# Kernel optimization log

Measured on AMD Instinct MI355X. Metric: run time of the kernel, lower is better.

The kernel has to match this reference:

```python
import jax, jax.numpy as jnp
import numpy as np

B, N, E = 2, 2048, 1024
H, D = 16, 64


def setup_inputs() -> dict:
    key = jax.random.key(0)
    k1, k2, k3 = jax.random.split(key, 3)
    x = jax.random.normal(k1, (B, N, E), dtype=jnp.float32)
    Wqkv = jax.random.normal(k2, (3 * H * D, E), dtype=jnp.float32) * 0.02
    bqkv = jnp.zeros((3 * H * D,), dtype=jnp.float32)
    Wout = jax.random.normal(k3, (E, H * D), dtype=jnp.float32) * 0.02
    bout = jnp.zeros((E,), dtype=jnp.float32)
    return {"x": x, "Wqkv": Wqkv, "bqkv": bqkv, "Wout": Wout, "bout": bout}


def reference(x, Wqkv, bqkv, Wout, bout):
    b, n, _ = x.shape
    scale = D ** (-0.5)
    # qkv projection: [b, n, 3*h*d], interpreted as (h, d, qkv) per einops pattern
    qkv = (x @ Wqkv.T + bqkv).reshape(b, n, H, D, 3)
    q = jnp.transpose(qkv[..., 0], (0, 2, 1, 3))  # [b, h, n, d]
    k = jnp.transpose(qkv[..., 1], (0, 2, 1, 3))
    v = jnp.transpose(qkv[..., 2], (0, 2, 1, 3))
    att = jnp.einsum('bhid,bhjd->bhij', q, k) * scale  # [b, h, n, n]
    causal = jnp.tril(jnp.ones((n, n), dtype=bool))
    att = jnp.where(causal, att, -jnp.inf)
    att = jax.nn.softmax(att, axis=-1)
    out = jnp.einsum('bhij,bhjd->bhid', att, v)  # [b, h, n, d]
    out = jnp.transpose(out, (0, 2, 1, 3)).reshape(b, n, H * D)
    return out @ Wout.T + bout
```

## Files before the change

### kernel.cpp

```cpp
#include <hip/hip_runtime.h>
#include <hip/hip_bf16.h>

#define B_ 2
#define N_ 2048
#define E_ 1024
#define H_ 16
#define D_ 64
#define M_ 4096
#define HD_ 1024
#define NT_ 3072

using f32x4  = __attribute__((ext_vector_type(4))) float;
using f32x16 = __attribute__((ext_vector_type(16))) float;
using bf16x8 = __attribute__((ext_vector_type(8))) short;

static __device__ __forceinline__ unsigned short f2bf(float f) {
  union { float f; unsigned u; } v; v.f = f;
  unsigned r = v.u + 0x7FFF + ((v.u >> 16) & 1);
  return (unsigned short)(r >> 16);
}
static __device__ __forceinline__ float bf2f(short s) {
  union { unsigned u; float f; } v; v.u = ((unsigned)(unsigned short)s) << 16; return v.f;
}

static __device__ __forceinline__ void gld16(const void* g, void* l) {
  __builtin_amdgcn_global_load_lds(
      (const __attribute__((address_space(1))) unsigned int*)g,
      (__attribute__((address_space(3))) unsigned int*)l, 16, 0, 0);
}

static __device__ __forceinline__ unsigned cvtpk(float lo, float hi) {
  unsigned r;
  asm("v_cvt_pk_bf16_f32 %0, %1, %2" : "=v"(r) : "v"(lo), "v"(hi));
  return r;
}
static __device__ __forceinline__ void pl32swap(unsigned& a, unsigned& b) {
  asm("v_permlane32_swap_b32 %0, %1" : "+v"(a), "+v"(b));
}

static __device__ __forceinline__ int gswz(int row) {
  return ((row >> 1) & 3) ^ ((row >> 3) & 1);
}


__global__ void k_cvt_x(const float* __restrict__ x, unsigned short* __restrict__ xb) {
  int t = blockIdx.x * 256 + threadIdx.x;
  float4 v = reinterpret_cast<const float4*>(x)[t];
  ushort4 o;
  o.x = f2bf(v.x); o.y = f2bf(v.y); o.z = f2bf(v.z); o.w = f2bf(v.w);
  reinterpret_cast<ushort4*>(xb)[t] = o;
}

__global__ void k_cvt_wqkv(const float* __restrict__ w, const float* __restrict__ bsrc,
                           unsigned short* __restrict__ wb, float* __restrict__ br) {
  int t = blockIdx.x * 256 + threadIdx.x;
  int r = t >> 8;
  int c = (t & 255) * 4;
  int kind = r >> 10, hd = r & 1023;
  int h = hd >> 6, d = hd & 63;
  int rin = h * 192 + d * 3 + kind;
  float s = (kind == 0) ? 0.125f * 1.4426950408889634f : 1.0f;
  float4 v = *reinterpret_cast<const float4*>(w + (size_t)rin * E_ + c);
  ushort4 o;
  o.x = f2bf(v.x * s); o.y = f2bf(v.y * s); o.z = f2bf(v.z * s); o.w = f2bf(v.w * s);
  *reinterpret_cast<ushort4*>(wb + (size_t)r * E_ + c) = o;
  if (c == 0) br[r] = bsrc[rin] * s;
}

__global__ void k_cvt_wout(const float* __restrict__ w, unsigned short* __restrict__ wb) {
  int t = blockIdx.x * 256 + threadIdx.x;
  int r = t >> 8;
  int c = (t & 255) * 4;
  float4 v = *reinterpret_cast<const float4*>(w + (size_t)r * HD_ + c);
  ushort4 o;
  o.x = f2bf(v.x); o.y = f2bf(v.y); o.z = f2bf(v.z); o.w = f2bf(v.w);
  *reinterpret_cast<ushort4*>(wb + (size_t)r * HD_ + c) = o;
}

template <int EPI, int BM>
__global__ __launch_bounds__(256, 2) void k_gemm(
    const unsigned short* __restrict__ A,
    const unsigned short* __restrict__ W,
    const float* __restrict__ bias,
    unsigned short* __restrict__ Qo, unsigned short* __restrict__ Ko,
    unsigned short* __restrict__ Vo, float* __restrict__ Fo,
    int M, int Nt, int K)
{
  constexpr int APT = (BM == 128) ? 2 : 1;
  constexpr int NF  = (BM == 128) ? 4 : 2;
  __shared__ unsigned short As[3][BM * 32];
  __shared__ unsigned short Bs[3][128 * 32];
  const int t = threadIdx.x;
  const int w = t >> 6, l = t & 63, lg = l >> 4, lr = l & 15;
  const int wrow0 = (BM == 128) ? (w >> 1) * 64 : 0;
  const int wcol0 = (BM == 128) ? (w & 1) * 64 : w * 32;
  const int row0 = blockIdx.x * BM, col0 = blockIdx.y * 128;
  const int NT = K >> 5;

  f32x4 acc[4][NF] = {};

  auto stage = [&](int b, int k0) {
#pragma unroll
    for (int c = 0; c < APT; ++c) {
      int ci = w * APT + c;
      int row = ci * 16 + (l >> 2);
      int sub = (l & 3) ^ gswz(row);
      gld16(A + (size_t)(row0 + row) * K + k0 + sub * 8,
            (unsigned short*)&As[b][0] + ci * 512);
    }
#pragma unroll
    for (int c = 0; c < 2; ++c) {
      int ci = w * 2 + c;
      int row = ci * 16 + (l >> 2);
      int sub = (l & 3) ^ gswz(row);
      gld16(W + (size_t)(col0 + row) * K + k0 + sub * 8,
            (unsigned short*)&Bs[b][0] + ci * 512);
    }
  };

  stage(0, 0);
  stage(1, 32);

  for (int kt = 0; kt < NT; ++kt) {
    const int ib = kt % 3;
    if (kt + 1 < NT) {
      if constexpr (BM == 128) asm volatile("s_waitcnt vmcnt(4)" ::: "memory");
      else                     asm volatile("s_waitcnt vmcnt(3)" ::: "memory");
    } else {
      asm volatile("s_waitcnt vmcnt(0)" ::: "memory");
    }
    asm volatile("s_barrier" ::: "memory");
    if (kt + 2 < NT) stage((kt + 2) % 3, (kt + 2) * 32);

    bf16x8 af[4], bf[NF];
#pragma unroll
    for (int m = 0; m < 4; ++m) {
      int row = wrow0 + m * 16 + lr;
      af[m] = *reinterpret_cast<const bf16x8*>(
          &As[ib][row * 32 + ((lg ^ gswz(row)) * 8)]);
    }
#pragma unroll
    for (int n = 0; n < NF; ++n) {
      int row = wcol0 + n * 16 + lr;
      bf[n] = *reinterpret_cast<const bf16x8*>(
          &Bs[ib][row * 32 + ((lg ^ gswz(row)) * 8)]);
    }
    __builtin_amdgcn_s_setprio(1);
#pragma unroll
    for (int m = 0; m < 4; ++m)
#pragma unroll
      for (int n = 0; n < NF; ++n)
        acc[m][n] = __builtin_amdgcn_mfma_f32_16x16x32_bf16(af[m], bf[n], acc[m][n], 0, 0, 0);
    __builtin_amdgcn_s_setprio(0);
  }

#pragma unroll
  for (int m = 0; m < 4; ++m) {
#pragma unroll
    for (int n = 0; n < NF; ++n) {
      int col = col0 + wcol0 + n * 16 + lr;
      float bb = bias[col];
#pragma unroll
      for (int rr = 0; rr < 4; ++rr) {
        int ro = row0 + wrow0 + m * 16 + lg * 4 + rr;
        float val = acc[m][n][rr] + bb;
        if (EPI == 0) {
          int kind = col >> 10, hd = col & 1023, h = hd >> 6, d = hd & 63;
          int bi = ro >> 11, ni = ro & 2047;
          unsigned short bv = f2bf(val);
          size_t bh = (size_t)(bi * H_ + h);
          if (kind == 0)      Qo[(bh * N_ + ni) * D_ + d] = bv;
          else if (kind == 1) Ko[(bh * N_ + ni) * D_ + d] = bv;
          else                Vo[bh * (size_t)(D_ * N_) + (size_t)d * N_ + ni] = bv;
        } else {
          Fo[(size_t)ro * HD_ + col] = val;
        }
      }
    }
  }
}

__global__ __launch_bounds__(256, 3) void k_attn(
    const unsigned short* __restrict__ Q,
    const unsigned short* __restrict__ Kg,
    const unsigned short* __restrict__ Vg,
    unsigned short* __restrict__ O,
    unsigned short* __restrict__ Pp,
    float* __restrict__ Pml)
{
  static const int u_qt[24] = {15,15,14,13,12,11,10, 9,   8, 7,14, 6,13, 5,12, 4,   8, 0, 9, 1,10, 2,11, 3};
  static const int u_t0[24] = { 0,16, 0, 0, 0, 0, 0, 0,   0, 0,16, 0,16, 0,16, 0,  16, 0,16, 0,16, 0,16, 0};
  static const int u_ps[24] = {14,15,12,10, 8, 6, 4, 2,   0,-1,13,-1,11,-1, 9,-1,   1,-1, 3,-1, 5,-1, 7,-1};

  __shared__ alignas(16) unsigned short Ks[3][64 * 64];
  __shared__ alignas(16) unsigned short Vs[3][64 * 64];

  const int t = threadIdx.x;
  const int w = t >> 6, l = t & 63;
  const int lq = l & 31;
  const int hi = l >> 5;
  const int bh = blockIdx.x & 31;
  const int u  = blockIdx.x >> 5;
  const int qt = u_qt[u], t0 = u_t0[u], ps = u_ps[u];
  const int q0 = qt * 128;
  const int r0w = q0 + w * 32;
  const int rtop = r0w + 31;
  const bool splitc0 = (ps >= 0) && (t0 == 0);
  const int tendW = splitc0 ? 16 : ((rtop >> 6) + 1);
  const int tendB = splitc0 ? 16 : (((q0 + 127) >> 6) + 1);

  const unsigned short* Qb = Q  + (size_t)bh * (N_ * D_);
  const unsigned short* Kb = Kg + (size_t)bh * (N_ * D_);
  const unsigned short* Vb = Vg + (size_t)bh * (N_ * D_);

  const int pr  = l >> 3;
  const int pswz = ((l & 7) ^ pr) * 8;
  const unsigned short* KsrcB = Kb + pr * D_ + pswz;
  const unsigned short* VsrcB = Vb + pr * N_ + pswz;

  bf16x8 qf[4];
#pragma unroll
  for (int ks = 0; ks < 4; ++ks)
    qf[ks] = *reinterpret_cast<const bf16x8*>(
        Qb + (size_t)(r0w + lq) * D_ + ks * 16 + hi * 8);

  f32x16 oacc[2] = {};
  float lrun = 0.f;

  auto stage = [&](int b, int kt_) {
    const int kv = kt_ * 64;
#pragma unroll
    for (int c = 0; c < 2; ++c) {
      int cb = w * 2 + c;
      gld16(KsrcB + kv * D_ + cb * 512, (unsigned short*)&Ks[b][0] + cb * 512);
      gld16(VsrcB + kv + cb * 8 * N_,   (unsigned short*)&Vs[b][0] + cb * 512);
    }
  };

  stage(0, t0);
  if (t0 + 1 < tendB) stage(1, t0 + 1);

  for (int kt = t0; kt < tendB; ++kt) {
    const int ib = (kt - t0) % 3;
    if (kt + 1 < tendB) asm volatile("s_waitcnt vmcnt(4)" ::: "memory");
    else                asm volatile("s_waitcnt vmcnt(0)" ::: "memory");
    asm volatile("s_barrier" ::: "memory");
    if (kt + 2 < tendB) stage((kt - t0 + 2) % 3, kt + 2);

    if (kt < tendW) {
      const int kv0 = kt * 64;
      bf16x8 kf[2][4], vf[2][4];
#pragma unroll
      for (int ct = 0; ct < 2; ++ct)
#pragma unroll
        for (int ks = 0; ks < 4; ++ks) {
          int row = ct * 32 + lq;
          kf[ct][ks] = *reinterpret_cast<const bf16x8*>(
              &Ks[ib][row * 64 + (((ks * 2 + hi) ^ (lq & 7)) * 8)]);
        }
#pragma unroll
      for (int dt = 0; dt < 2; ++dt)
#pragma unroll
        for (int j = 0; j < 4; ++j) {
          int row = dt * 32 + lq;
          vf[dt][j] = *reinterpret_cast<const bf16x8*>(
              &Vs[ib][row * 64 + (((j * 2 + hi) ^ (lq & 7)) * 8)]);
        }

      f32x16 sct[2];
      __builtin_amdgcn_s_setprio(1);
#pragma unroll
      for (int ct = 0; ct < 2; ++ct) {
        f32x16 z = {};
#pragma unroll
        for (int ks = 0; ks < 4; ++ks)
          z = __builtin_amdgcn_mfma_f32_32x32x16_bf16(kf[ct][ks], qf[ks], z, 0, 0, 0);
        sct[ct] = z;
      }
      __builtin_amdgcn_s_setprio(0);

      if (kv0 + 63 > r0w) {
        int qrow = r0w + lq;
#pragma unroll
        for (int ct = 0; ct < 2; ++ct)
#pragma unroll
          for (int r = 0; r < 16; ++r) {
            int kv = kv0 + ct * 32 + (r & 3) + 8 * (r >> 2) + 4 * hi;
            if (kv > qrow) sct[ct][r] = -1e30f;
          }
      }

      float s16[16];
#pragma unroll
      for (int r = 0; r < 16; ++r) {
        float p0 = exp2f(sct[0][r]);
        float p1 = exp2f(sct[1][r]);
        sct[0][r] = p0; sct[1][r] = p1;
        s16[r] = p0 + p1;
      }
#pragma unroll
      for (int st = 8; st >= 1; st >>= 1)
#pragma unroll
        for (int r = 0; r < 8; ++r)
          if (r < st) s16[r] += s16[r + st];
      lrun += s16[0] + __shfl_xor(s16[0], 32);

      bf16x8 paf[4];
#pragma unroll
      for (int ct = 0; ct < 2; ++ct) {
        unsigned u0 = cvtpk(sct[ct][0],  sct[ct][1]);
        unsigned u1 = cvtpk(sct[ct][2],  sct[ct][3]);
        unsigned u2 = cvtpk(sct[ct][4],  sct[ct][5]);
        unsigned u3 = cvtpk(sct[ct][6],  sct[ct][7]);
        unsigned u4 = cvtpk(sct[ct][8],  sct[ct][9]);
        unsigned u5 = cvtpk(sct[ct][10], sct[ct][11]);
        unsigned u6 = cvtpk(sct[ct][12], sct[ct][13]);
        unsigned u7 = cvtpk(sct[ct][14], sct[ct][15]);
        pl32swap(u0, u2); pl32swap(u1, u3);
        pl32swap(u4, u6); pl32swap(u5, u7);
        union { unsigned uu[4]; bf16x8 v; } c0, c1;
        c0.uu[0] = u0; c0.uu[1] = u1; c0.uu[2] = u2; c0.uu[3] = u3;
        c1.uu[0] = u4; c1.uu[1] = u5; c1.uu[2] = u6; c1.uu[3] = u7;
        paf[ct * 2]     = c0.v;
        paf[ct * 2 + 1] = c1.v;
      }

      __builtin_amdgcn_s_setprio(1);
#pragma unroll
      for (int dt = 0; dt < 2; ++dt)
#pragma unroll
        for (int j = 0; j < 4; ++j)
          oacc[dt] = __builtin_amdgcn_mfma_f32_32x32x16_bf16(paf[j], vf[dt][j], oacc[dt], 0, 0, 0);
      __builtin_amdgcn_s_setprio(0);
    }
  }

  int bi = bh >> 4, h = bh & 15;
  if (ps < 0) {
    float inv = 1.0f / lrun;
    float iv[16];
#pragma unroll
    for (int r = 0; r < 16; ++r)
      iv[r] = __shfl(inv, (r & 3) + 8 * (r >> 2) + 4 * hi);
#pragma unroll
    for (int dt = 0; dt < 2; ++dt)
#pragma unroll
      for (int r = 0; r < 16; ++r) {
        int qr = r0w + (r & 3) + 8 * (r >> 2) + 4 * hi;
        int d = dt * 32 + lq;
        O[((size_t)(bi * N_ + qr) * H_ + h) * D_ + d] = f2bf(oacc[dt][r] * iv[r]);
      }
  } else {
    unsigned short* pb = Pp + (size_t)(bh * 16 + ps) * (128 * 64);
    float* mb = Pml + (size_t)(bh * 16 + ps) * 128;
#pragma unroll
    for (int dt = 0; dt < 2; ++dt)
#pragma unroll
      for (int r = 0; r < 16; ++r) {
        int rloc = w * 32 + (r & 3) + 8 * (r >> 2) + 4 * hi;
        pb[rloc * 64 + dt * 32 + lq] = f2bf(oacc[dt][r]);
      }
    if (l < 32) {
      int rloc = w * 32 + l;
      mb[rloc] = lrun;
    }
  }
}

__global__ void k_merge(const unsigned short* __restrict__ Pp,
                        const float* __restrict__ Pml,
                        unsigned short* __restrict__ O) {
  int t = blockIdx.x * 256 + threadIdx.x;
  int dseg = t & 7;
  int rloc = (t >> 3) & 127;
  int qt8 = (t >> 10) & 7;
  int bh  = t >> 13;
  size_t b0 = (size_t)(bh * 16 + qt8 * 2) * 128 + rloc;
  size_t b1 = b0 + 128;
  bf16x8 o0 = *reinterpret_cast<const bf16x8*>(Pp + b0 * 64 + dseg * 8);
  bf16x8 o1 = *reinterpret_cast<const bf16x8*>(Pp + b1 * 64 + dseg * 8);
  float l0 = Pml[b0], l1 = Pml[b1];
  float inv = 1.0f / (l0 + l1);
  int n = (qt8 + 8) * 128 + rloc;
  int bi = bh >> 4, h = bh & 15;
  unsigned short* op = O + ((size_t)(bi * N_ + n) * H_ + h) * D_ + dseg * 8;
  bf16x8 res;
#pragma unroll
  for (int j = 0; j < 8; ++j)
    res[j] = (short)f2bf((bf2f(o0[j]) + bf2f(o1[j])) * inv);
  *reinterpret_cast<bf16x8*>(op) = res;
}


extern "C" void kernel_launch(void* const* d_in, const int* in_sizes, int n_in,
                              void* d_out, int out_size, void* d_ws, size_t ws_size,
                              hipStream_t stream) {
  const float* x    = (const float*)d_in[0];
  const float* Wqkv = (const float*)d_in[1];
  const float* bqkv = (const float*)d_in[2];
  const float* Wout = (const float*)d_in[3];
  const float* bout = (const float*)d_in[4];
  float* out = (float*)d_out;

  char* ws = (char*)d_ws;
  unsigned short* xb  = (unsigned short*)ws; ws += (size_t)M_ * E_ * 2;
  unsigned short* wqb = (unsigned short*)ws; ws += (size_t)NT_ * E_ * 2;
  float*          bqr = (float*)ws;          ws += 16384;
  unsigned short* wob = (unsigned short*)ws; ws += (size_t)E_ * HD_ * 2;
  unsigned short* Qb  = (unsigned short*)ws; ws += (size_t)M_ * D_ * H_ * 2;
  unsigned short* Kb  = (unsigned short*)ws; ws += (size_t)M_ * D_ * H_ * 2;
  unsigned short* Vb  = (unsigned short*)ws; ws += (size_t)M_ * D_ * H_ * 2;
  unsigned short* ao  = (unsigned short*)ws; ws += (size_t)M_ * HD_ * 2;

  unsigned short* Pp  = xb;
  float*          Pml = (float*)wqb;

  k_cvt_x<<<(M_ * E_) / 4 / 256, 256, 0, stream>>>(x, xb);
  k_cvt_wqkv<<<NT_, 256, 0, stream>>>(Wqkv, bqkv, wqb, bqr);
  k_cvt_wout<<<E_, 256, 0, stream>>>(Wout, wob);

  k_gemm<0, 128><<<dim3(M_ / 128, NT_ / 128), 256, 0, stream>>>(
      xb, wqb, bqr, Qb, Kb, Vb, nullptr, M_, NT_, E_);

  k_attn<<<768, 256, 0, stream>>>(Qb, Kb, Vb, ao, Pp, Pml);
  k_merge<<<1024, 256, 0, stream>>>(Pp, Pml, ao);

  k_gemm<1, 64><<<dim3(M_ / 64, HD_ / 128), 256, 0, stream>>>(
      ao, wob, bout, nullptr, nullptr, nullptr, out, M_, HD_, E_);
}
```

Measured before the change: 118.8 us.

## Use 2-wave blocks with larger per-wave tiles in QKV GEMM and attention

Adds a dedicated QKV projection GEMM that runs 128 threads per block, where each wave computes a 128x64 tile with 8x4 MFMA accumulators. The attention kernel likewise drops to 2 waves per block, with each wave handling 64 query rows (two 32-row groups) against every K/V tile it loads. Each wave therefore gets more reuse from every LDS fragment read. The cost is higher register pressure and fewer waves per CU for hiding latency, and each thread issues more global-to-LDS loads per stage.

```diff
diff --git a/kernel.cpp b/kernel.cpp
--- a/kernel.cpp
+++ b/kernel.cpp
@@ -75,6 +75,96 @@
   ushort4 o;
   o.x = f2bf(v.x); o.y = f2bf(v.y); o.z = f2bf(v.z); o.w = f2bf(v.w);
   *reinterpret_cast<ushort4*>(wb + (size_t)r * HD_ + c) = o;
+}
+
+__global__ __launch_bounds__(128, 2) void k_gemm0(
+    const unsigned short* __restrict__ A,
+    const unsigned short* __restrict__ W,
+    const float* __restrict__ bias,
+    unsigned short* __restrict__ Qo, unsigned short* __restrict__ Ko,
+    unsigned short* __restrict__ Vo)
+{
+  __shared__ unsigned short As[3][128 * 32];
+  __shared__ unsigned short Bs[3][128 * 32];
+  const int t = threadIdx.x;
+  const int w = t >> 6, l = t & 63, lg = l >> 4, lr = l & 15;
+  const int row0 = blockIdx.x * 128, col0 = blockIdx.y * 128;
+  constexpr int K = 1024;
+  constexpr int NT = K >> 5;
+
+  f32x4 acc[8][4] = {};
+
+  auto stage = [&](int b, int k0) {
+#pragma unroll
+    for (int c = 0; c < 4; ++c) {
+      int ci = w * 4 + c;
+      int row = ci * 16 + (l >> 2);
+      int sub = (l & 3) ^ gswz(row);
+      gld16(A + (size_t)(row0 + row) * K + k0 + sub * 8,
+            (unsigned short*)&As[b][0] + ci * 512);
+    }
+#pragma unroll
+    for (int c = 0; c < 4; ++c) {
+      int ci = w * 4 + c;
+      int row = ci * 16 + (l >> 2);
+      int sub = (l & 3) ^ gswz(row);
+      gld16(W + (size_t)(col0 + row) * K + k0 + sub * 8,
+            (unsigned short*)&Bs[b][0] + ci * 512);
+    }
+  };
+
+  stage(0, 0);
+  stage(1, 32);
+
+  for (int kt = 0; kt < NT; ++kt) {
+    const int ib = kt % 3;
+    if (kt + 1 < NT) asm volatile("s_waitcnt vmcnt(8)" ::: "memory");
+    else             asm volatile("s_waitcnt vmcnt(0)" ::: "memory");
+    asm volatile("s_barrier" ::: "memory");
+    if (kt + 2 < NT) stage((kt + 2) % 3, (kt + 2) * 32);
+
+    bf16x8 af[8], bf[4];
+#pragma unroll
+    for (int m = 0; m < 8; ++m) {
+      int row = m * 16 + lr;
+      af[m] = *reinterpret_cast<const bf16x8*>(
+          &As[ib][row * 32 + ((lg ^ gswz(row)) * 8)]);
+    }
+#pragma unroll
+    for (int n = 0; n < 4; ++n) {
+      int row = w * 64 + n * 16 + lr;
+      bf[n] = *reinterpret_cast<const bf16x8*>(
+          &Bs[ib][row * 32 + ((lg ^ gswz(row)) * 8)]);
+    }
+    __builtin_amdgcn_s_setprio(1);
+#pragma unroll
+    for (int m = 0; m < 8; ++m)
+#pragma unroll
+      for (int n = 0; n < 4; ++n)
+        acc[m][n] = __builtin_amdgcn_mfma_f32_16x16x32_bf16(af[m], bf[n], acc[m][n], 0, 0, 0);
+    __builtin_amdgcn_s_setprio(0);
+  }
+
+  const int kind = col0 >> 10;
+#pragma unroll
+  for (int m = 0; m < 8; ++m) {
+#pragma unroll
+    for (int n = 0; n < 4; ++n) {
+      int col = col0 + w * 64 + n * 16 + lr;
+      float bb = bias[col];
+      int hd = col & 1023, h = hd >> 6, d = hd & 63;
+#pragma unroll
+      for (int rr = 0; rr < 4; ++rr) {
+        int ro = row0 + m * 16 + lg * 4 + rr;
+        int bi = ro >> 11, ni = ro & 2047;
+        unsigned short bv = f2bf(acc[m][n][rr] + bb);
+        size_t bh = (size_t)(bi * H_ + h);
+        if (kind == 0)      Qo[(bh * N_ + ni) * D_ + d] = bv;
+        else if (kind == 1) Ko[(bh * N_ + ni) * D_ + d] = bv;
+        else                Vo[bh * (size_t)(D_ * N_) + (size_t)d * N_ + ni] = bv;
+      }
+    }
+  }
 }
 
 template <int EPI, int BM>
@@ -164,15 +254,7 @@
       for (int rr = 0; rr < 4; ++rr) {
         int ro = row0 + wrow0 + m * 16 + lg * 4 + rr;
         float val = acc[m][n][rr] + bb;
-        if (EPI == 0) {
-          int kind = col >> 10, hd = col & 1023, h = hd >> 6, d = hd & 63;
-          int bi = ro >> 11, ni = ro & 2047;
-          unsigned short bv = f2bf(val);
-          size_t bh = (size_t)(bi * H_ + h);
-          if (kind == 0)      Qo[(bh * N_ + ni) * D_ + d] = bv;
-          else if (kind == 1) Ko[(bh * N_ + ni) * D_ + d] = bv;
-          else                Vo[bh * (size_t)(D_ * N_) + (size_t)d * N_ + ni] = bv;
-        } else {
+        if (EPI == 1) {
           Fo[(size_t)ro * HD_ + col] = val;
         }
       }
@@ -180,7 +262,7 @@
   }
 }
 
-__global__ __launch_bounds__(256, 3) void k_attn(
+__global__ __launch_bounds__(128, 2) void k_attn(
     const unsigned short* __restrict__ Q,
     const unsigned short* __restrict__ Kg,
     const unsigned short* __restrict__ Vg,
@@ -203,8 +285,8 @@
   const int u  = blockIdx.x >> 5;
   const int qt = u_qt[u], t0 = u_t0[u], ps = u_ps[u];
   const int q0 = qt * 128;
-  const int r0w = q0 + w * 32;
-  const int rtop = r0w + 31;
+  const int r0w = q0 + w * 64;
+  const int rtop = r0w + 63;
   const bool splitc0 = (ps >= 0) && (t0 == 0);
   const int tendW = splitc0 ? 16 : ((rtop >> 6) + 1);
   const int tendB = splitc0 ? 16 : (((q0 + 127) >> 6) + 1);
@@ -218,20 +300,22 @@
   const unsigned short* KsrcB = Kb + pr * D_ + pswz;
   const unsigned short* VsrcB = Vb + pr * N_ + pswz;
 
-  bf16x8 qf[4];
-#pragma unroll
-  for (int ks = 0; ks < 4; ++ks)
-    qf[ks] = *reinterpret_cast<const bf16x8*>(
-        Qb + (size_t)(r0w + lq) * D_ + ks * 16 + hi * 8);
-
-  f32x16 oacc[2] = {};
-  float lrun = 0.f;
+  bf16x8 qf[2][4];
+#pragma unroll
+  for (int rg = 0; rg < 2; ++rg)
+#pragma unroll
+    for (int ks = 0; ks < 4; ++ks)
+      qf[rg][ks] = *reinterpret_cast<const bf16x8*>(
+          Qb + (size_t)(r0w + rg * 32 + lq) * D_ + ks * 16 + hi * 8);
+
+  f32x16 oacc[2][2] = {};
+  float lrun[2] = {0.f, 0.f};
 
   auto stage = [&](int b, int kt_) {
     const int kv = kt_ * 64;
 #pragma unroll
-    for (int c = 0; c < 2; ++c) {
-      int cb = w * 2 + c;
+    for (int c = 0; c < 4; ++c) {
+      int cb = w * 4 + c;
       gld16(KsrcB + kv * D_ + cb * 512, (unsigned short*)&Ks[b][0] + cb * 512);
       gld16(VsrcB + kv + cb * 8 * N_,   (unsigned short*)&Vs[b][0] + cb * 512);
     }
@@ -242,7 +326,7 @@
 
   for (int kt = t0; kt < tendB; ++kt) {
     const int ib = (kt - t0) % 3;
-    if (kt + 1 < tendB) asm volatile("s_waitcnt vmcnt(4)" ::: "memory");
+    if (kt + 1 < tendB) asm volatile("s_waitcnt vmcnt(8)" ::: "memory");
     else                asm volatile("s_waitcnt vmcnt(0)" ::: "memory");
     asm volatile("s_barrier" ::: "memory");
     if (kt + 2 < tendB) stage((kt - t0 + 2) % 3, kt + 2);
@@ -267,102 +351,108 @@
               &Vs[ib][row * 64 + (((j * 2 + hi) ^ (lq & 7)) * 8)]);
         }
 
-      f32x16 sct[2];
-      __builtin_amdgcn_s_setprio(1);
-#pragma unroll
-      for (int ct = 0; ct < 2; ++ct) {
-        f32x16 z = {};
-#pragma unroll
-        for (int ks = 0; ks < 4; ++ks)
-          z = __builtin_amdgcn_mfma_f32_32x32x16_bf16(kf[ct][ks], qf[ks], z, 0, 0, 0);
-        sct[ct] = z;
+#pragma unroll
+      for (int rg = 0; rg < 2; ++rg) {
+        f32x16 sct[2];
+        __builtin_amdgcn_s_setprio(1);
+#pragma unroll
+        for (int ct = 0; ct < 2; ++ct) {
+          f32x16 z = {};
+#pragma unroll
+          for (int ks = 0; ks < 4; ++ks)
+            z = __builtin_amdgcn_mfma_f32_32x32x16_bf16(kf[ct][ks], qf[rg][ks], z, 0, 0, 0);
+          sct[ct] = z;
+        }
+        __builtin_amdgcn_s_setprio(0);
+
+        int qrow = r0w + rg * 32 + lq;
+        if (kv0 + 63 > qrow - (int)lq) {
+#pragma unroll
+          for (int ct = 0; ct < 2; ++ct)
+#pragma unroll
+            for (int r = 0; r < 16; ++r) {
+              int kv = kv0 + ct * 32 + (r & 3) + 8 * (r >> 2) + 4 * hi;
+              if (kv > qrow) sct[ct][r] = -1e30f;
+            }
+        }
+
+        float s16[16];
+#pragma unroll
+        for (int r = 0; r < 16; ++r) {
+          float p0 = exp2f(sct[0][r]);
+          float p1 = exp2f(sct[1][r]);
+          sct[0][r] = p0; sct[1][r] = p1;
+          s16[r] = p0 + p1;
+        }
+#pragma unroll
+        for (int st = 8; st >= 1; st >>= 1)
+#pragma unroll
+          for (int r = 0; r < 8; ++r)
+            if (r < st) s16[r] += s16[r + st];
+        lrun[rg] += s16[0] + __shfl_xor(s16[0], 32);
+
+        bf16x8 paf[4];
+#pragma unroll
+        for (int ct = 0; ct < 2; ++ct) {
+          unsigned u0 = cvtpk(sct[ct][0],  sct[ct][1]);
+          unsigned u1 = cvtpk(sct[ct][2],  sct[ct][3]);
+          unsigned u2 = cvtpk(sct[ct][4],  sct[ct][5]);
+          unsigned u3 = cvtpk(sct[ct][6],  sct[ct][7]);
+          unsigned u4 = cvtpk(sct[ct][8],  sct[ct][9]);
+          unsigned u5 = cvtpk(sct[ct][10], sct[ct][11]);
+          unsigned u6 = cvtpk(sct[ct][12], sct[ct][13]);
+          unsigned u7 = cvtpk(sct[ct][14], sct[ct][15]);
+          pl32swap(u0, u2); pl32swap(u1, u3);
+          pl32swap(u4, u6); pl32swap(u5, u7);
+          union { unsigned uu[4]; bf16x8 v; } c0, c1;
+          c0.uu[0] = u0; c0.uu[1] = u1; c0.uu[2] = u2; c0.uu[3] = u3;
+          c1.uu[0] = u4; c1.uu[1] = u5; c1.uu[2] = u6; c1.uu[3] = u7;
+          paf[ct * 2]     = c0.v;
+          paf[ct * 2 + 1] = c1.v;
+        }
+
+        __builtin_amdgcn_s_setprio(1);
+#pragma unroll
+        for (int dt = 0; dt < 2; ++dt)
+#pragma unroll
+          for (int j = 0; j < 4; ++j)
+            oacc[rg][dt] = __builtin_amdgcn_mfma_f32_32x32x16_bf16(paf[j], vf[dt][j], oacc[rg][dt], 0, 0, 0);
+        __builtin_amdgcn_s_setprio(0);
       }
-      __builtin_amdgcn_s_setprio(0);
-
-      if (kv0 + 63 > r0w) {
-        int qrow = r0w + lq;
-#pragma unroll
-        for (int ct = 0; ct < 2; ++ct)
-#pragma unroll
-          for (int r = 0; r < 16; ++r) {
-            int kv = kv0 + ct * 32 + (r & 3) + 8 * (r >> 2) + 4 * hi;
-            if (kv > qrow) sct[ct][r] = -1e30f;
-          }
-      }
-
-      float s16[16];
-#pragma unroll
-      for (int r = 0; r < 16; ++r) {
-        float p0 = exp2f(sct[0][r]);
-        float p1 = exp2f(sct[1][r]);
-        sct[0][r] = p0; sct[1][r] = p1;
-        s16[r] = p0 + p1;
-      }
-#pragma unroll
-      for (int st = 8; st >= 1; st >>= 1)
-#pragma unroll
-        for (int r = 0; r < 8; ++r)
-          if (r < st) s16[r] += s16[r + st];
-      lrun += s16[0] + __shfl_xor(s16[0], 32);
-
-      bf16x8 paf[4];
-#pragma unroll
-      for (int ct = 0; ct < 2; ++ct) {
-        unsigned u0 = cvtpk(sct[ct][0],  sct[ct][1]);
-        unsigned u1 = cvtpk(sct[ct][2],  sct[ct][3]);
-        unsigned u2 = cvtpk(sct[ct][4],  sct[ct][5]);
-        unsigned u3 = cvtpk(sct[ct][6],  sct[ct][7]);
-        unsigned u4 = cvtpk(sct[ct][8],  sct[ct][9]);
-        unsigned u5 = cvtpk(sct[ct][10], sct[ct][11]);
-        unsigned u6 = cvtpk(sct[ct][12], sct[ct][13]);
-        unsigned u7 = cvtpk(sct[ct][14], sct[ct][15]);
-        pl32swap(u0, u2); pl32swap(u1, u3);
-        pl32swap(u4, u6); pl32swap(u5, u7);
-        union { unsigned uu[4]; bf16x8 v; } c0, c1;
-        c0.uu[0] = u0; c0.uu[1] = u1; c0.uu[2] = u2; c0.uu[3] = u3;
-        c1.uu[0] = u4; c1.uu[1] = u5; c1.uu[2] = u6; c1.uu[3] = u7;
-        paf[ct * 2]     = c0.v;
-        paf[ct * 2 + 1] = c1.v;
-      }
-
-      __builtin_amdgcn_s_setprio(1);
-#pragma unroll
-      for (int dt = 0; dt < 2; ++dt)
-#pragma unroll
-        for (int j = 0; j < 4; ++j)
-          oacc[dt] = __builtin_amdgcn_mfma_f32_32x32x16_bf16(paf[j], vf[dt][j], oacc[dt], 0, 0, 0);
-      __builtin_amdgcn_s_setprio(0);
     }
   }
 
   int bi = bh >> 4, h = bh & 15;
   if (ps < 0) {
-    float inv = 1.0f / lrun;
-    float iv[16];
-#pragma unroll
-    for (int r = 0; r < 16; ++r)
-      iv[r] = __shfl(inv, (r & 3) + 8 * (r >> 2) + 4 * hi);
-#pragma unroll
-    for (int dt = 0; dt < 2; ++dt)
-#pragma unroll
-      for (int r = 0; r < 16; ++r) {
-        int qr = r0w + (r & 3) + 8 * (r >> 2) + 4 * hi;
-        int d = dt * 32 + lq;
-        O[((size_t)(bi * N_ + qr) * H_ + h) * D_ + d] = f2bf(oacc[dt][r] * iv[r]);
-      }
+#pragma unroll
+    for (int rg = 0; rg < 2; ++rg) {
+      float inv = 1.0f / lrun[rg];
+      float iv[16];
+#pragma unroll
+      for (int r = 0; r < 16; ++r)
+        iv[r] = __shfl(inv, (r & 3) + 8 * (r >> 2) + 4 * hi + (l & 32));
+#pragma unroll
+      for (int dt = 0; dt < 2; ++dt)
+#pragma unroll
+        for (int r = 0; r < 16; ++r) {
+          int qr = r0w + rg * 32 + (r & 3) + 8 * (r >> 2) + 4 * hi;
+          int d = dt * 32 + lq;
+          O[((size_t)(bi * N_ + qr) * H_ + h) * D_ + d] = f2bf(oacc[rg][dt][r] * iv[r]);
+        }
+    }
   } else {
     unsigned short* pb = Pp + (size_t)(bh * 16 + ps) * (128 * 64);
     float* mb = Pml + (size_t)(bh * 16 + ps) * 128;
 #pragma unroll
-    for (int dt = 0; dt < 2; ++dt)
-#pragma unroll
-      for (int r = 0; r < 16; ++r) {
-        int rloc = w * 32 + (r & 3) + 8 * (r >> 2) + 4 * hi;
-        pb[rloc * 64 + dt * 32 + lq] = f2bf(oacc[dt][r]);
-      }
-    if (l < 32) {
-      int rloc = w * 32 + l;
-      mb[rloc] = lrun;
+    for (int rg = 0; rg < 2; ++rg) {
+#pragma unroll
+      for (int dt = 0; dt < 2; ++dt)
+#pragma unroll
+        for (int r = 0; r < 16; ++r) {
+          int rloc = w * 64 + rg * 32 + (r & 3) + 8 * (r >> 2) + 4 * hi;
+          pb[rloc * 64 + dt * 32 + lq] = f2bf(oacc[rg][dt][r]);
+        }
+      if (l < 32) mb[w * 64 + rg * 32 + l] = lrun[rg];
     }
   }
 }
@@ -419,10 +509,10 @@
   k_cvt_wqkv<<<NT_, 256, 0, stream>>>(Wqkv, bqkv, wqb, bqr);
   k_cvt_wout<<<E_, 256, 0, stream>>>(Wout, wob);
 
-  k_gemm<0, 128><<<dim3(M_ / 128, NT_ / 128), 256, 0, stream>>>(
-      xb, wqb, bqr, Qb, Kb, Vb, nullptr, M_, NT_, E_);
-
-  k_attn<<<768, 256, 0, stream>>>(Qb, Kb, Vb, ao, Pp, Pml);
+  k_gemm0<<<dim3(M_ / 128, NT_ / 128), 128, 0, stream>>>(
+      xb, wqb, bqr, Qb, Kb, Vb);
+
+  k_attn<<<768, 128, 0, stream>>>(Qb, Kb, Vb, ao, Pp, Pml);
   k_merge<<<1024, 256, 0, stream>>>(Pp, Pml, ao);
 
   k_gemm<1, 64><<<dim3(M_ / 64, HD_ / 128), 256, 0, stream>>>(
```

Result: slower. 138.9 us (+16.9%).
